# Performance work log

Hardware: AMD Instinct MI355X
Metric: run time of the kernel (lower is better)

The kernel has to match this reference:

```python
import jax, jax.numpy as jnp
import numpy as np

TARGET = 560   # target_size
EPS = 1e-8


def setup_inputs() -> dict:
    key = jax.random.key(0)
    k1, k2, k3, k4 = jax.random.split(key, 4)
    B, K, D, C, N = 2, 1600, 1024, 256, 32
    feats = jax.random.normal(k1, (B, K, D), dtype=jnp.float32)
    embedding = jax.random.normal(k2, (C, D), dtype=jnp.float32)
    # valid boxes: x_min,y_min in [0, 400), side in [16, 160) => min_box_size satisfied, in-bounds
    xy_min = jax.random.randint(k3, (B, N, 2), 0, TARGET - 160)
    wh = jax.random.randint(k4, (B, N, 2), 16, 160)
    xy_max = jnp.minimum(xy_min + wh, TARGET)
    boxes = jnp.concatenate([xy_min, xy_max], axis=-1).astype(jnp.int32)  # (B,N,4) = x_min,y_min,x_max,y_max
    return {"feats": feats, "embedding": embedding, "boxes": boxes}


def reference(feats, embedding, boxes):
    # feats: (B,K,D) patch features, embedding: (C,D) class prototypes, boxes: (B,N,4) int
    B, K, D = feats.shape
    C = embedding.shape[0]
    P = int(np.sqrt(K))  # patch_2d_size

    # --- get_cosim_mini_batch (normalize=True), fused as a single GEMM + norm ---
    dot = jnp.einsum('bkd,cd->bck', feats, embedding)          # (B,C,K)
    feats_norm = jnp.linalg.norm(feats, axis=-1)               # (B,K)
    emb_norm = jnp.linalg.norm(embedding, axis=-1)             # (C,)
    cosim = dot / (feats_norm[:, None, :] * emb_norm[None, :, None] + EPS)
    cosim = cosim.reshape(B, C, P, P)
    cosim = jax.image.resize(cosim, (B, C, TARGET, TARGET), method='bicubic')  # (B,C,560,560)
    # single scale -> stack().mean(0) is identity

    # --- box mean pooling: cosim[b,:,y_min:y_max-1, x_min:x_max-1].mean((1,2)) via masks ---
    x_min, y_min, x_max, y_max = boxes[..., 0], boxes[..., 1], boxes[..., 2], boxes[..., 3]
    r = jnp.arange(TARGET)
    my = ((r[None, None, :] >= y_min[..., None]) & (r[None, None, :] <= y_max[..., None] - 2)).astype(cosim.dtype)  # (B,N,H)
    mx = ((r[None, None, :] >= x_min[..., None]) & (r[None, None, :] <= x_max[..., None] - 2)).astype(cosim.dtype)  # (B,N,W)
    counts = my.sum(-1) * mx.sum(-1)                           # (B,N)
    pooled = jnp.einsum('bnh,bnw,bchw->bnc', my, mx, cosim)    # (B,N,C)
    box_sim = pooled / counts[..., None]
    return box_sim.reshape(-1, C)
```

## Files before the change

kernel.cpp:

```cpp
#include <hip/hip_runtime.h>
#include <hip/hip_bf16.h>
#include <math.h>

#define TGT 560
#define B_ 2
#define K_ 1600
#define D_ 1024
#define C_ 256
#define N_ 32
#define P_ 40
#define KC_ 32
#define KCHUNK 50

#define OFF_W   ((size_t)0)
#define OFF_IFN (OFF_W + (size_t)TGT * P_)
#define OFF_IEN (OFF_IFN + (size_t)B_ * K_)
#define OFF_V   (OFF_IEN + (size_t)C_)
#define OFF_GP  (OFF_V + (size_t)B_ * N_ * K_)

__global__ __launch_bounds__(256) void k1_norms_w(const float* __restrict__ feats,
                                                  const float* __restrict__ emb,
                                                  float* __restrict__ ws) {
    __shared__ float red[4];
    const int r = blockIdx.x;
    const int t = threadIdx.x;
    if (r < B_ * K_ + C_) {
        const float* src;
        float* dst;
        if (r < B_ * K_) { src = feats + (size_t)r * D_; dst = ws + OFF_IFN + r; }
        else             { src = emb + (size_t)(r - B_ * K_) * D_; dst = ws + OFF_IEN + (r - B_ * K_); }
        float4 v = ((const float4*)src)[t];
        float s = v.x * v.x + v.y * v.y + v.z * v.z + v.w * v.w;
        #pragma unroll
        for (int off = 32; off > 0; off >>= 1) s += __shfl_down(s, off, 64);
        if ((t & 63) == 0) red[t >> 6] = s;
        __syncthreads();
        if (t == 0) {
            float tot = red[0] + red[1] + red[2] + red[3];
            *dst = 1.0f / sqrtf(tot);
        }
    } else {
        int idx = (r - (B_ * K_ + C_)) * 256 + t;
        if (idx < TGT * P_) {
            int h = idx / P_;
            int p = idx - h * P_;
            float sf = ((float)h + 0.5f) * (1.0f / 14.0f) - 0.5f;
            int jf = (int)floorf(sf);
            float norm = 0.f, wp = 0.f;
            #pragma unroll
            for (int dj = -1; dj <= 2; ++dj) {
                int j = jf + dj;
                if (j < 0 || j >= P_) continue;
                float x = fabsf(sf - (float)j);
                float w = ((1.5f * x - 2.5f) * x) * x + 1.f;
                if (x >= 1.f) w = ((-0.5f * x + 2.5f) * x - 4.f) * x + 2.f;
                if (x >= 2.f) w = 0.f;
                norm += w;
                if (j == p) wp = w;
            }
            ws[OFF_W + idx] = wp / norm;
        }
    }
}

__global__ __launch_bounds__(256) void k2_boxw(const int* __restrict__ boxes,
                                               float* __restrict__ ws) {
    __shared__ float part[256];
    __shared__ float wxy[80];
    const int bn = blockIdx.x;
    const int b = bn >> 5, n = bn & 31;
    const int t = threadIdx.x;
    const int* bx = boxes + bn * 4;
    const int xmin = bx[0], ymin = bx[1], xmax = bx[2], ymax = bx[3];
    const float invcnt = 1.0f / ((float)(ymax - 1 - ymin) * (float)(xmax - 1 - xmin));

    const int axis = t >> 7;
    const int rr = t & 127;
    const int p = rr % 40;
    const int slice = rr / 40;
    float partial = 0.f;
    if (rr < 120) {
        int lo = (axis ? xmin : ymin) + slice;
        int hi = (axis ? xmax : ymax) - 2;
        const float* Wp = ws + OFF_W;
        for (int h = lo; h <= hi; h += 3) partial += Wp[h * P_ + p];
    }
    part[t] = partial;
    __syncthreads();
    if (t < 80) {
        int a = t / 40, pp = t % 40;
        int base = a * 128;
        wxy[t] = part[base + pp] + part[base + 40 + pp] + part[base + 80 + pp];
    }
    __syncthreads();
    const float* ifn = ws + OFF_IFN + (size_t)b * K_;
    float* v = ws + OFF_V + ((size_t)b * N_ + n) * K_;
    for (int k = t; k < K_; k += 256) {
        int pq = k / P_;
        int q = k - pq * P_;
        v[k] = wxy[pq] * wxy[40 + q] * ifn[k] * invcnt;
    }
}

__global__ __launch_bounds__(256) void k3_gp(const float* __restrict__ feats,
                                             const float* __restrict__ wsv,
                                             float* __restrict__ gp) {
    __shared__ float vlds[KCHUNK * N_];
    const int bid = blockIdx.x;
    const int b = bid >> 7;
    const int rest = bid & 127;
    const int kc = rest >> 2;
    const int dt = rest & 3;
    const int t = threadIdx.x;
    const int k0 = kc * KCHUNK;

    for (int i = t; i < KCHUNK * N_; i += 256) {
        int n = i / KCHUNK;
        int kk = i - n * KCHUNK;
        vlds[kk * N_ + n] = wsv[((size_t)b * N_ + n) * K_ + k0 + kk];
    }
    __syncthreads();

    float acc[N_];
    #pragma unroll
    for (int n = 0; n < N_; ++n) acc[n] = 0.f;

    const float* fp = feats + ((size_t)b * K_ + k0) * D_ + dt * 256 + t;
    #pragma unroll 2
    for (int kk = 0; kk < KCHUNK; ++kk) {
        float f = fp[(size_t)kk * D_];
        #pragma unroll
        for (int n = 0; n < N_; ++n) acc[n] = fmaf(vlds[kk * N_ + n], f, acc[n]);
    }
    float* o = gp + (((size_t)b * KC_ + kc) * N_) * D_ + dt * 256 + t;
    #pragma unroll
    for (int n = 0; n < N_; ++n) o[(size_t)n * D_] = acc[n];
}

__global__ __launch_bounds__(256) void k4_out(const float* __restrict__ emb,
                                              const float* __restrict__ gp,
                                              const float* __restrict__ ien,
                                              float* __restrict__ out) {
    __shared__ float4 g4[D_ / 4];
    __shared__ float part[256];
    const int bid = blockIdx.x;
    const int bn = bid >> 2;
    const int ct = bid & 3;
    const int b = bn >> 5, n = bn & 31;
    const int t = threadIdx.x;

    float4 a = {0.f, 0.f, 0.f, 0.f};
    #pragma unroll 4
    for (int kc = 0; kc < KC_; ++kc) {
        const float4* src = (const float4*)gp + (((size_t)b * KC_ + kc) * N_ + n) * (D_ / 4) + t;
        float4 x = *src;
        a.x += x.x; a.y += x.y; a.z += x.z; a.w += x.w;
    }
    g4[t] = a;
    __syncthreads();

    const int cl = t & 63;
    const int dq = t >> 6;
    const int c = ct * 64 + cl;
    const float4* e4 = (const float4*)(emb + (size_t)c * D_) + dq * 64;
    const float4* gg = g4 + dq * 64;
    float partial = 0.f;
    #pragma unroll 8
    for (int i = 0; i < 64; ++i) {
        float4 e = e4[i];
        float4 g = gg[i];
        partial += e.x * g.x + e.y * g.y + e.z * g.z + e.w * g.w;
    }
    part[t] = partial;
    __syncthreads();
    if (t < 64) {
        int c2 = ct * 64 + t;
        float val = part[t] + part[64 + t] + part[128 + t] + part[192 + t];
        out[(size_t)bn * C_ + c2] = val * ien[c2];
    }
}

extern "C" void kernel_launch(void* const* d_in, const int* in_sizes, int n_in,
                              void* d_out, int out_size, void* d_ws, size_t ws_size,
                              hipStream_t stream) {
    const float* feats = (const float*)d_in[0];
    const float* emb   = (const float*)d_in[1];
    const int*   boxes = (const int*)d_in[2];
    float* out = (float*)d_out;
    float* ws  = (float*)d_ws;

    const int norm_blocks = B_ * K_ + C_;
    const int w_blocks = (TGT * P_ + 255) / 256;
    k1_norms_w<<<norm_blocks + w_blocks, 256, 0, stream>>>(feats, emb, ws);
    k2_boxw<<<B_ * N_, 256, 0, stream>>>(boxes, ws);
    k3_gp<<<B_ * KC_ * 4, 256, 0, stream>>>(feats, ws + OFF_V, ws + OFF_GP);
    k4_out<<<B_ * N_ * 4, 256, 0, stream>>>(emb, ws + OFF_GP, ws + OFF_IEN, out);
}
```

Baseline: 109.3 us.

## Fuse box-weight computation into norm kernel and build v on the fly in GEMV

Drops the separate box-weight kernel. Each box now computes its per-axis bicubic weight sums directly by scattering into shared memory with atomics, with no precomputed 560x40 weight table. The second kernel rebuilds the per-box v vector from those 80 weights and the inverse feature norms in shared memory instead of reading a materialised v array. Its inner loop batches 10 feature loads and reads v as float4. This saves one launch and some global traffic, at the cost of LDS atomics and redundant v construction in every block.

```diff
diff --git a/kernel.cpp b/kernel.cpp
--- a/kernel.cpp
+++ b/kernel.cpp
@@ -12,16 +12,16 @@
 #define KC_ 32
 #define KCHUNK 50
 
-#define OFF_W   ((size_t)0)
-#define OFF_IFN (OFF_W + (size_t)TGT * P_)
+#define OFF_IFN ((size_t)0)
 #define OFF_IEN (OFF_IFN + (size_t)B_ * K_)
-#define OFF_V   (OFF_IEN + (size_t)C_)
-#define OFF_GP  (OFF_V + (size_t)B_ * N_ * K_)
+#define OFF_BOXW (OFF_IEN + (size_t)C_)
+#define OFF_GP  ((size_t)16384)
 
-__global__ __launch_bounds__(256) void k1_norms_w(const float* __restrict__ feats,
-                                                  const float* __restrict__ emb,
-                                                  float* __restrict__ ws) {
-    __shared__ float red[4];
+__global__ __launch_bounds__(256) void kA(const float* __restrict__ feats,
+                                          const float* __restrict__ emb,
+                                          const int* __restrict__ boxes,
+                                          float* __restrict__ ws) {
+    __shared__ float shm[80];
     const int r = blockIdx.x;
     const int t = threadIdx.x;
     if (r < B_ * K_ + C_) {
@@ -33,78 +33,59 @@
         float s = v.x * v.x + v.y * v.y + v.z * v.z + v.w * v.w;
         #pragma unroll
         for (int off = 32; off > 0; off >>= 1) s += __shfl_down(s, off, 64);
-        if ((t & 63) == 0) red[t >> 6] = s;
+        if ((t & 63) == 0) shm[t >> 6] = s;
         __syncthreads();
         if (t == 0) {
-            float tot = red[0] + red[1] + red[2] + red[3];
+            float tot = shm[0] + shm[1] + shm[2] + shm[3];
             *dst = 1.0f / sqrtf(tot);
         }
     } else {
-        int idx = (r - (B_ * K_ + C_)) * 256 + t;
-        if (idx < TGT * P_) {
-            int h = idx / P_;
-            int p = idx - h * P_;
+        const int bn = r - (B_ * K_ + C_);
+        if (t < 80) shm[t] = 0.f;
+        __syncthreads();
+        const int* bx = boxes + bn * 4;
+        const int xmin = bx[0], ymin = bx[1], xmax = bx[2], ymax = bx[3];
+        const float invcnt = 1.0f / ((float)(ymax - 1 - ymin) * (float)(xmax - 1 - xmin));
+        const int axis = t >> 7;
+        const int rr = t & 127;
+        const int lo = (axis ? xmin : ymin);
+        const int hi = (axis ? xmax : ymax) - 2;
+        for (int h = lo + rr; h <= hi; h += 128) {
             float sf = ((float)h + 0.5f) * (1.0f / 14.0f) - 0.5f;
             int jf = (int)floorf(sf);
-            float norm = 0.f, wp = 0.f;
+            float w[4];
+            float norm = 0.f;
             #pragma unroll
             for (int dj = -1; dj <= 2; ++dj) {
                 int j = jf + dj;
-                if (j < 0 || j >= P_) continue;
                 float x = fabsf(sf - (float)j);
-                float w = ((1.5f * x - 2.5f) * x) * x + 1.f;
-                if (x >= 1.f) w = ((-0.5f * x + 2.5f) * x - 4.f) * x + 2.f;
-                if (x >= 2.f) w = 0.f;
-                norm += w;
-                if (j == p) wp = w;
+                float wv = ((1.5f * x - 2.5f) * x) * x + 1.f;
+                if (x >= 1.f) wv = ((-0.5f * x + 2.5f) * x - 4.f) * x + 2.f;
+                if (x >= 2.f) wv = 0.f;
+                if (j < 0 || j >= P_) wv = 0.f;
+                w[dj + 1] = wv;
+                norm += wv;
             }
-            ws[OFF_W + idx] = wp / norm;
+            float inv = 1.0f / norm;
+            #pragma unroll
+            for (int dj = 0; dj < 4; ++dj) {
+                int j = jf - 1 + dj;
+                if (w[dj] != 0.f) atomicAdd(&shm[axis * P_ + j], w[dj] * inv);
+            }
+        }
+        __syncthreads();
+        if (t < 80) {
+            float val = shm[t];
+            if (t < P_) val *= invcnt;
+            ws[OFF_BOXW + (size_t)bn * 80 + t] = val;
         }
     }
 }
 
-__global__ __launch_bounds__(256) void k2_boxw(const int* __restrict__ boxes,
-                                               float* __restrict__ ws) {
-    __shared__ float part[256];
-    __shared__ float wxy[80];
-    const int bn = blockIdx.x;
-    const int b = bn >> 5, n = bn & 31;
-    const int t = threadIdx.x;
-    const int* bx = boxes + bn * 4;
-    const int xmin = bx[0], ymin = bx[1], xmax = bx[2], ymax = bx[3];
-    const float invcnt = 1.0f / ((float)(ymax - 1 - ymin) * (float)(xmax - 1 - xmin));
-
-    const int axis = t >> 7;
-    const int rr = t & 127;
-    const int p = rr % 40;
-    const int slice = rr / 40;
-    float partial = 0.f;
-    if (rr < 120) {
-        int lo = (axis ? xmin : ymin) + slice;
-        int hi = (axis ? xmax : ymax) - 2;
-        const float* Wp = ws + OFF_W;
-        for (int h = lo; h <= hi; h += 3) partial += Wp[h * P_ + p];
-    }
-    part[t] = partial;
-    __syncthreads();
-    if (t < 80) {
-        int a = t / 40, pp = t % 40;
-        int base = a * 128;
-        wxy[t] = part[base + pp] + part[base + 40 + pp] + part[base + 80 + pp];
-    }
-    __syncthreads();
-    const float* ifn = ws + OFF_IFN + (size_t)b * K_;
-    float* v = ws + OFF_V + ((size_t)b * N_ + n) * K_;
-    for (int k = t; k < K_; k += 256) {
-        int pq = k / P_;
-        int q = k - pq * P_;
-        v[k] = wxy[pq] * wxy[40 + q] * ifn[k] * invcnt;
-    }
-}
-
-__global__ __launch_bounds__(256) void k3_gp(const float* __restrict__ feats,
-                                             const float* __restrict__ wsv,
-                                             float* __restrict__ gp) {
+__global__ __launch_bounds__(256) void kB(const float* __restrict__ feats,
+                                          const float* __restrict__ ws,
+                                          float* __restrict__ gp) {
+    __shared__ float sw[N_ * 80];
     __shared__ float vlds[KCHUNK * N_];
     const int bid = blockIdx.x;
     const int b = bid >> 7;
@@ -114,10 +95,16 @@
     const int t = threadIdx.x;
     const int k0 = kc * KCHUNK;
 
+    for (int i = t; i < N_ * 80; i += 256)
+        sw[i] = ws[OFF_BOXW + (size_t)b * N_ * 80 + i];
+    __syncthreads();
+    const float* ifn = ws + OFF_IFN + (size_t)b * K_;
     for (int i = t; i < KCHUNK * N_; i += 256) {
-        int n = i / KCHUNK;
-        int kk = i - n * KCHUNK;
-        vlds[kk * N_ + n] = wsv[((size_t)b * N_ + n) * K_ + k0 + kk];
+        int kk = i >> 5, n = i & 31;
+        int k = k0 + kk;
+        int pq = k / P_;
+        int q = k - pq * P_;
+        vlds[kk * N_ + n] = sw[n * 80 + pq] * sw[n * 80 + P_ + q] * ifn[k];
     }
     __syncthreads();
 
@@ -126,21 +113,33 @@
     for (int n = 0; n < N_; ++n) acc[n] = 0.f;
 
     const float* fp = feats + ((size_t)b * K_ + k0) * D_ + dt * 256 + t;
-    #pragma unroll 2
-    for (int kk = 0; kk < KCHUNK; ++kk) {
-        float f = fp[(size_t)kk * D_];
+    #pragma unroll
+    for (int g = 0; g < 5; ++g) {
+        float f[10];
         #pragma unroll
-        for (int n = 0; n < N_; ++n) acc[n] = fmaf(vlds[kk * N_ + n], f, acc[n]);
+        for (int u = 0; u < 10; ++u) f[u] = fp[(size_t)(g * 10 + u) * D_];
+        #pragma unroll
+        for (int u = 0; u < 10; ++u) {
+            const float4* vp = (const float4*)&vlds[(g * 10 + u) * N_];
+            #pragma unroll
+            for (int j = 0; j < 8; ++j) {
+                float4 v4 = vp[j];
+                acc[4 * j + 0] = fmaf(v4.x, f[u], acc[4 * j + 0]);
+                acc[4 * j + 1] = fmaf(v4.y, f[u], acc[4 * j + 1]);
+                acc[4 * j + 2] = fmaf(v4.z, f[u], acc[4 * j + 2]);
+                acc[4 * j + 3] = fmaf(v4.w, f[u], acc[4 * j + 3]);
+            }
+        }
     }
     float* o = gp + (((size_t)b * KC_ + kc) * N_) * D_ + dt * 256 + t;
     #pragma unroll
     for (int n = 0; n < N_; ++n) o[(size_t)n * D_] = acc[n];
 }
 
-__global__ __launch_bounds__(256) void k4_out(const float* __restrict__ emb,
-                                              const float* __restrict__ gp,
-                                              const float* __restrict__ ien,
-                                              float* __restrict__ out) {
+__global__ __launch_bounds__(256) void kC(const float* __restrict__ emb,
+                                          const float* __restrict__ gp,
+                                          const float* __restrict__ ien,
+                                          float* __restrict__ out) {
     __shared__ float4 g4[D_ / 4];
     __shared__ float part[256];
     const int bid = blockIdx.x;
@@ -189,10 +188,7 @@
     float* out = (float*)d_out;
     float* ws  = (float*)d_ws;
 
-    const int norm_blocks = B_ * K_ + C_;
-    const int w_blocks = (TGT * P_ + 255) / 256;
-    k1_norms_w<<<norm_blocks + w_blocks, 256, 0, stream>>>(feats, emb, ws);
-    k2_boxw<<<B_ * N_, 256, 0, stream>>>(boxes, ws);
-    k3_gp<<<B_ * KC_ * 4, 256, 0, stream>>>(feats, ws + OFF_V, ws + OFF_GP);
-    k4_out<<<B_ * N_ * 4, 256, 0, stream>>>(emb, ws + OFF_GP, ws + OFF_IEN, out);
+    kA<<<B_ * K_ + C_ + B_ * N_, 256, 0, stream>>>(feats, emb, boxes, ws);
+    kB<<<B_ * KC_ * 4, 256, 0, stream>>>(feats, ws, ws + OFF_GP);
+    kC<<<B_ * N_ * 4, 256, 0, stream>>>(emb, ws + OFF_GP, ws + OFF_IEN, out);
 }
```

After: 96.52 us. 11.7% less time.
